# Kernel tuning notes

Hardware: AMD Instinct MI355X
Metric: run time of the kernel (lower is better)

## Reference

```python
import jax, jax.numpy as jnp
import numpy as np

N = 100000   # nodes
E = 1200000  # edges
D = 64       # emb_dim
XIN = 18     # x_dim + node_dim
XD = 16      # x_dim (output)
ED = 1       # edge_dim
L = 4        # num message-passing layers
G = 8        # graphs in batch (for global_mean_pool)


def setup_inputs() -> dict:
    key = jax.random.key(0)
    ks = iter(jax.random.split(key, 64))
    def nrm(shape, s=0.05):
        return jax.random.normal(next(ks), shape, dtype=jnp.float32) * s
    inp = {}
    inp["x"] = jax.random.normal(next(ks), (N, XIN), dtype=jnp.float32)
    inp["edge_attr"] = jax.random.normal(next(ks), (E, ED), dtype=jnp.float32)
    inp["W_in"] = nrm((XIN, D)); inp["b_in"] = jnp.zeros((D,), jnp.float32)
    # per-layer stacked params (leading dim L)
    inp["msg_W1"] = nrm((L, 2 * D + ED, D)); inp["msg_b1"] = jnp.zeros((L, D), jnp.float32)
    inp["msg_g1"] = jnp.ones((L, D), jnp.float32); inp["msg_be1"] = jnp.zeros((L, D), jnp.float32)
    inp["msg_W2"] = nrm((L, D, D)); inp["msg_b2"] = jnp.zeros((L, D), jnp.float32)
    inp["msg_g2"] = jnp.ones((L, D), jnp.float32); inp["msg_be2"] = jnp.zeros((L, D), jnp.float32)
    inp["upd_W1"] = nrm((L, 2 * D, D)); inp["upd_b1"] = jnp.zeros((L, D), jnp.float32)
    inp["upd_g1"] = jnp.ones((L, D), jnp.float32); inp["upd_be1"] = jnp.zeros((L, D), jnp.float32)
    inp["upd_W2"] = nrm((L, D, D)); inp["upd_b2"] = jnp.zeros((L, D), jnp.float32)
    inp["upd_g2"] = jnp.ones((L, D), jnp.float32); inp["upd_be2"] = jnp.zeros((L, D), jnp.float32)
    inp["reward_W"] = nrm((D, D)); inp["reward_b"] = jnp.zeros((D,), jnp.float32)
    inp["rout_W"] = nrm((D, 1)); inp["rout_b"] = jnp.zeros((1,), jnp.float32)
    inp["pred_W"] = nrm((D, D)); inp["pred_b"] = jnp.zeros((D,), jnp.float32)
    inp["pout_W"] = nrm((D, XD)); inp["pout_b"] = jnp.zeros((XD,), jnp.float32)
    inp["edge_index"] = jax.random.randint(next(ks), (2, E), 0, N)
    inp["batch"] = jnp.sort(jax.random.randint(next(ks), (N,), 0, G))
    return inp


def _bn(x, g, b, eps=1e-5):
    # BatchNorm1d in training mode: batch mean + biased variance
    m = jnp.mean(x, axis=0)
    v = jnp.mean((x - m) ** 2, axis=0)
    return (x - m) * jax.lax.rsqrt(v + eps) * g + b


def _mlp(x, W1, b1, g1, be1, W2, b2, g2, be2):
    h = jax.nn.relu(_bn(x @ W1 + b1, g1, be1))
    return jax.nn.relu(_bn(h @ W2 + b2, g2, be2))


def _forward(x, edge_attr, W_in, b_in,
             msg_W1, msg_b1, msg_g1, msg_be1, msg_W2, msg_b2, msg_g2, msg_be2,
             upd_W1, upd_b1, upd_g1, upd_be1, upd_W2, upd_b2, upd_g2, upd_be2,
             reward_W, reward_b, rout_W, rout_b, pred_W, pred_b, pout_W, pout_b,
             edge_index, batch):
    src = edge_index[0]  # j (source)
    dst = edge_index[1]  # i (target); PyG default flow source_to_target
    n = x.shape[0]
    h = x @ W_in + b_in
    for l in range(L):
        # message: gather + concat + MLP(psi)
        m = jnp.concatenate([h[dst], h[src], edge_attr], axis=-1)  # (E, 2D+ED)
        m = _mlp(m, msg_W1[l], msg_b1[l], msg_g1[l], msg_be1[l],
                 msg_W2[l], msg_b2[l], msg_g2[l], msg_be2[l])
        # aggregate: scatter-add to target nodes
        agg = jax.ops.segment_sum(m, dst, num_segments=n)  # (N, D)
        # update: concat + MLP(phi); residual add from outer network
        u = jnp.concatenate([h, agg], axis=-1)
        h = h + _mlp(u, upd_W1[l], upd_b1[l], upd_g1[l], upd_be1[l],
                     upd_W2[l], upd_b2[l], upd_g2[l], upd_be2[l])
    # reward head (computed in the original forward but not returned)
    h_reward = h @ reward_W + reward_b
    cnt = jax.ops.segment_sum(jnp.ones((n,), h.dtype), batch, num_segments=G)
    h_graph = jax.ops.segment_sum(h_reward, batch, num_segments=G) / jnp.maximum(cnt, 1.0)[:, None]
    _out_reward = h_graph @ rout_W + rout_b  # unused, matches original return
    # prediction head
    x_out = jax.nn.relu(h @ pred_W + pred_b) @ pout_W + pout_b  # (N, XD)
    return x_out


def reference(x, edge_attr, W_in, b_in,
              msg_W1, msg_b1, msg_g1, msg_be1, msg_W2, msg_b2, msg_g2, msg_be2,
              upd_W1, upd_b1, upd_g1, upd_be1, upd_W2, upd_b2, upd_g2, upd_be2,
              reward_W, reward_b, rout_W, rout_b, pred_W, pred_b, pout_W, pout_b,
              edge_index, batch):
    return _forward(x, edge_attr, W_in, b_in,
                    msg_W1, msg_b1, msg_g1, msg_be1, msg_W2, msg_b2, msg_g2, msg_be2,
                    upd_W1, upd_b1, upd_g1, upd_be1, upd_W2, upd_b2, upd_g2, upd_be2,
                    reward_W, reward_b, rout_W, rout_b, pred_W, pred_b, pout_W, pout_b,
                    edge_index, batch)
```

## Files before the change

### kernel.cpp

```cpp
#include <hip/hip_runtime.h>
#include <hip/hip_fp16.h>

typedef unsigned short u16;
typedef unsigned int u32;
typedef __attribute__((ext_vector_type(8))) unsigned short us8;
typedef __attribute__((ext_vector_type(8))) _Float16 f16x8;
typedef __attribute__((ext_vector_type(4))) float f32x4;

#define EPS 1e-5f

__device__ __forceinline__ float h2f(u16 h){ __half v; *(u16*)&v = h; return __half2float(v); }
__device__ __forceinline__ u16 f2h(float f){ __half v = __float2half(f); return *(u16*)&v; }

__global__ __launch_bounds__(256) void k_in(const float* __restrict__ x,
    const float* __restrict__ Win, const float* __restrict__ bin,
    float* __restrict__ h, int N){
  __shared__ float Ws[18][64];
  __shared__ float xs[64][20];
  int tid = threadIdx.x;
  for (int i = tid; i < 18*64; i += 256) Ws[i>>6][i&63] = Win[i];
  int row0 = blockIdx.x * 64;
  for (int i = tid; i < 64*18; i += 256){
    int r = i/18, k = i - r*18;
    int row = row0 + r;
    xs[r][k] = (row < N) ? x[(size_t)row*18 + k] : 0.f;
  }
  __syncthreads();
  int rq = tid >> 4, dq = tid & 15;
  float4 b4 = *(const float4*)(bin + dq*4);
  float acc[4][4];
  #pragma unroll
  for (int j=0;j<4;j++){ acc[j][0]=b4.x; acc[j][1]=b4.y; acc[j][2]=b4.z; acc[j][3]=b4.w; }
  for (int k=0;k<18;k++){
    float4 wv = *(const float4*)&Ws[k][dq*4];
    #pragma unroll
    for (int j=0;j<4;j++){
      float v = xs[rq*4+j][k];
      acc[j][0]+=v*wv.x; acc[j][1]+=v*wv.y; acc[j][2]+=v*wv.z; acc[j][3]+=v*wv.w;
    }
  }
  #pragma unroll
  for (int j=0;j<4;j++){
    int row = row0 + rq*4 + j;
    if (row < N)
      *(float4*)(h + (size_t)row*64 + dq*4) = make_float4(acc[j][0],acc[j][1],acc[j][2],acc[j][3]);
  }
}

__global__ __launch_bounds__(256) void k_pq(const float* __restrict__ h,
    const float* __restrict__ A, const float* __restrict__ B,
    u16* __restrict__ P, u16* __restrict__ Q, int N){
  __shared__ float hs[64][68];
  __shared__ float As[64][64];
  __shared__ float Bs[64][64];
  int tid = threadIdx.x;
  for (int i = tid; i < 4096; i += 256){ As[i>>6][i&63] = A[i]; Bs[i>>6][i&63] = B[i]; }
  int row0 = blockIdx.x*64;
  for (int i = tid; i < 4096; i += 256){
    int r = i>>6, k = i&63; int row = row0+r;
    hs[r][k] = (row<N)? h[(size_t)row*64+k] : 0.f;
  }
  __syncthreads();
  int rq = tid>>4, dq = tid&15;
  float ap[4][4]={}, aq[4][4]={};
  for (int k=0;k<64;k+=4){
    float4 hv[4];
    #pragma unroll
    for (int j=0;j<4;j++) hv[j] = *(const float4*)&hs[rq*4+j][k];
    #pragma unroll
    for (int kk=0;kk<4;kk++){
      float4 av = *(const float4*)&As[k+kk][dq*4];
      float4 bv = *(const float4*)&Bs[k+kk][dq*4];
      #pragma unroll
      for (int j=0;j<4;j++){
        float v = ((const float*)&hv[j])[kk];
        ap[j][0]+=v*av.x; ap[j][1]+=v*av.y; ap[j][2]+=v*av.z; ap[j][3]+=v*av.w;
        aq[j][0]+=v*bv.x; aq[j][1]+=v*bv.y; aq[j][2]+=v*bv.z; aq[j][3]+=v*bv.w;
      }
    }
  }
  #pragma unroll
  for (int j=0;j<4;j++){
    int row = row0 + rq*4 + j;
    if (row<N){
      ushort4 pk, qk;
      pk.x=f2h(ap[j][0]); pk.y=f2h(ap[j][1]); pk.z=f2h(ap[j][2]); pk.w=f2h(ap[j][3]);
      qk.x=f2h(aq[j][0]); qk.y=f2h(aq[j][1]); qk.z=f2h(aq[j][2]); qk.w=f2h(aq[j][3]);
      *(ushort4*)(P+(size_t)row*64+dq*4) = pk;
      *(ushort4*)(Q+(size_t)row*64+dq*4) = qk;
    }
  }
}

__global__ __launch_bounds__(256) void k_hist(const int* __restrict__ ei, int* __restrict__ cnt, int E){
  int e = blockIdx.x*256 + threadIdx.x;
  if (e < E) atomicAdd(&cnt[ei[E+e]], 1);
}

__global__ __launch_bounds__(256) void k_scan_a(const int* __restrict__ cnt, int* __restrict__ rp,
    int* __restrict__ bsum, int N){
  __shared__ int sm[256];
  int tid = threadIdx.x;
  int i0 = blockIdx.x*1024 + tid*4;
  int v0 = (i0+0<N)? cnt[i0+0]:0;
  int v1 = (i0+1<N)? cnt[i0+1]:0;
  int v2 = (i0+2<N)? cnt[i0+2]:0;
  int v3 = (i0+3<N)? cnt[i0+3]:0;
  int s = v0+v1+v2+v3;
  sm[tid] = s; __syncthreads();
  for (int ofs=1; ofs<256; ofs<<=1){
    int v = sm[tid];
    if (tid >= ofs) v += sm[tid-ofs];
    __syncthreads(); sm[tid] = v; __syncthreads();
  }
  int base = sm[tid] - s;
  int a0 = base+v0, a1 = a0+v1, a2 = a1+v2, a3 = a2+v3;
  if (i0+0<N) rp[i0+0]=a0;
  if (i0+1<N) rp[i0+1]=a1;
  if (i0+2<N) rp[i0+2]=a2;
  if (i0+3<N) rp[i0+3]=a3;
  if (tid==255) bsum[blockIdx.x] = sm[255];
}

__global__ void k_scan_b(int* __restrict__ bsum, int NB){
  if (threadIdx.x==0){
    int run = 0;
    for (int b=0;b<NB;b++){ int t = bsum[b]; bsum[b] = run; run += t; }
  }
}

__global__ __launch_bounds__(256) void k_scan_c(const int* __restrict__ cnt, int* __restrict__ rp,
    int* __restrict__ wr, const int* __restrict__ bsum, int N, int E){
  int tid = threadIdx.x;
  int i0 = blockIdx.x*1024 + tid*4;
  int off = bsum[blockIdx.x];
  #pragma unroll
  for (int j=0;j<4;j++){
    int i = i0+j;
    if (i<N){ int ex = off + rp[i] - cnt[i]; rp[i] = ex; wr[i] = ex; }
  }
  if (blockIdx.x==0 && tid==0) rp[N] = E;
}

__global__ __launch_bounds__(256) void k_perm(const int* __restrict__ ei, const float* __restrict__ ea,
    int* __restrict__ wr, int* __restrict__ srcS, float* __restrict__ eaS, int E){
  int e = blockIdx.x*256 + threadIdx.x;
  if (e < E){
    int dn = ei[E+e];
    int pos = atomicAdd(&wr[dn], 1);
    srcS[pos] = ei[e];
    eaS[pos]  = ea[e];
  }
}

__global__ __launch_bounds__(256) void k_t1s(const u16* __restrict__ P, const u16* __restrict__ Q,
    const int* __restrict__ srcS, const float* __restrict__ eaS, const int* __restrict__ rp,
    const float* __restrict__ c1, const float* __restrict__ b1,
    u16* __restrict__ t, float* __restrict__ stats, int N){
  int tid = threadIdx.x;
  int d = tid & 63, w = tid >> 6;
  float cv = c1[d], bv = b1[d];
  float s = 0.f, sq = 0.f;
  for (int n = blockIdx.x*4 + w; n < N; n += gridDim.x*4){
    int a = rp[n], b = rp[n+1];
    float pv = h2f(P[(size_t)n*64 + d]) + bv;
    int p = a;
    for (; p + 1 < b; p += 2){
      int sn0 = srcS[p], sn1 = srcS[p+1];
      float ea0 = eaS[p], ea1 = eaS[p+1];
      float q0 = h2f(Q[(size_t)sn0*64 + d]);
      float q1 = h2f(Q[(size_t)sn1*64 + d]);
      float t0 = pv + q0 + ea0*cv;
      float t1 = pv + q1 + ea1*cv;
      t[(size_t)p*64 + d] = f2h(t0);
      t[(size_t)(p+1)*64 + d] = f2h(t1);
      s += t0 + t1; sq += t0*t0 + t1*t1;
    }
    if (p < b){
      int sn = srcS[p];
      float tt = pv + h2f(Q[(size_t)sn*64 + d]) + eaS[p]*cv;
      t[(size_t)p*64 + d] = f2h(tt);
      s += tt; sq += tt*tt;
    }
  }
  __shared__ float sS[4][64], qS[4][64];
  sS[w][d] = s; qS[w][d] = sq;
  __syncthreads();
  if (tid < 64){
    float ts = sS[0][tid]+sS[1][tid]+sS[2][tid]+sS[3][tid];
    float tq = qS[0][tid]+qS[1][tid]+qS[2][tid]+qS[3][tid];
    atomicAdd(&stats[tid], ts);
    atomicAdd(&stats[64+tid], tq);
  }
}

__global__ __launch_bounds__(256) void k_m2s(u16* __restrict__ t,
    const float* __restrict__ g1, const float* __restrict__ be1, const float* __restrict__ stats1,
    const float* __restrict__ W2, const float* __restrict__ b2,
    float* __restrict__ stats2, int E, float invE){
  __shared__ _Float16 yL[64][72];
  __shared__ _Float16 wL[64][72];
  __shared__ float scS[64], shS[64], b2S[64];
  int tid = threadIdx.x;
  if (tid < 64){
    float m = stats1[tid]*invE;
    float v = stats1[64+tid]*invE - m*m;
    float sc = g1[tid]*rsqrtf(v + EPS);
    scS[tid] = sc; shS[tid] = be1[tid] - m*sc;
    b2S[tid] = b2[tid];
  }
  for (int i = tid; i < 4096; i += 256){
    int k = i >> 6, n = i & 63;
    wL[n][k] = (_Float16)W2[i];
  }
  __syncthreads();
  int lane = tid & 63, wv = tid >> 6;
  int arow = lane & 15;
  int kgrp = lane >> 4;
  int srow = tid >> 2, sc0 = (tid & 3)*16;
  float ssum[4] = {}, ssq[4] = {};
  int ntiles = (E + 63) >> 6;
  for (int tile = blockIdx.x; tile < ntiles; tile += gridDim.x){
    int e0 = tile << 6;
    {
      int p = e0 + srow;
      f16x8 v0, v1;
      if (p < E){
        f16x8 a = *(const f16x8*)(t + (size_t)p*64 + sc0);
        f16x8 b = *(const f16x8*)(t + (size_t)p*64 + sc0 + 8);
        #pragma unroll
        for (int j=0;j<8;j++) v0[j] = (_Float16)fmaxf((float)a[j]*scS[sc0+j] + shS[sc0+j], 0.f);
        #pragma unroll
        for (int j=0;j<8;j++) v1[j] = (_Float16)fmaxf((float)b[j]*scS[sc0+8+j] + shS[sc0+8+j], 0.f);
      } else {
        #pragma unroll
        for (int j=0;j<8;j++){ v0[j] = (_Float16)0.f; v1[j] = (_Float16)0.f; }
      }
      *(f16x8*)&yL[srow][sc0]     = v0;
      *(f16x8*)&yL[srow][sc0 + 8] = v1;
    }
    __syncthreads();
    f16x8 a0 = *(const f16x8*)&yL[16*wv + arow][8*kgrp];
    f16x8 a1 = *(const f16x8*)&yL[16*wv + arow][32 + 8*kgrp];
    f32x4 acc[4];
    #pragma unroll
    for (int c=0;c<4;c++){
      f16x8 b0 = *(const f16x8*)&wL[16*c + arow][8*kgrp];
      f16x8 b1 = *(const f16x8*)&wL[16*c + arow][32 + 8*kgrp];
      f32x4 d = {0.f,0.f,0.f,0.f};
      d = __builtin_amdgcn_mfma_f32_16x16x32_f16(a0, b0, d, 0, 0, 0);
      d = __builtin_amdgcn_mfma_f32_16x16x32_f16(a1, b1, d, 0, 0, 0);
      acc[c] = d;
    }
    __syncthreads();
    #pragma unroll
    for (int c=0;c<4;c++){
      int col = 16*c + arow;
      float bb = b2S[col];
      #pragma unroll
      for (int r=0;r<4;r++){
        int e = e0 + 16*wv + kgrp*4 + r;
        if (e < E){
          float v = acc[c][r] + bb;
          t[(size_t)e*64 + col] = f2h(v);
          ssum[c] += v; ssq[c] += v*v;
        }
      }
    }
  }
  __syncthreads();
  float* red = (float*)yL;
  #pragma unroll
  for (int c=0;c<4;c++) red[c*256 + tid] = ssum[c];
  __syncthreads();
  if (tid < 64){
    int cc = tid >> 4;
    float s = 0.f;
    for (int g=0; g<16; g++) s += red[cc*256 + g*16 + (tid & 15)];
    atomicAdd(&stats2[tid], s);
  }
  __syncthreads();
  #pragma unroll
  for (int c=0;c<4;c++) red[c*256 + tid] = ssq[c];
  __syncthreads();
  if (tid < 64){
    int cc = tid >> 4;
    float s = 0.f;
    for (int g=0; g<16; g++) s += red[cc*256 + g*16 + (tid & 15)];
    atomicAdd(&stats2[64+tid], s);
  }
}

__global__ __launch_bounds__(256) void k_agg(const u16* __restrict__ t2, const int* __restrict__ rp,
    const float* __restrict__ g2, const float* __restrict__ be2, const float* __restrict__ stats2,
    float* __restrict__ agg, int N, float invE){
  __shared__ float scS[64], shS[64];
  int tid = threadIdx.x;
  if (tid < 64){
    float m = stats2[tid]*invE;
    float v = stats2[64+tid]*invE - m*m;
    float sc = g2[tid]*rsqrtf(v+EPS);
    scS[tid] = sc; shS[tid] = be2[tid] - m*sc;
  }
  __syncthreads();
  int lane = tid & 63, w = tid >> 6;
  float sc = scS[lane], sh = shS[lane];
  for (int n = blockIdx.x*4 + w; n < N; n += gridDim.x*4){
    int a = rp[n], b = rp[n+1];
    float acc = 0.f;
    for (int p = a; p < b; ++p){
      float v = h2f(t2[(size_t)p*64 + lane]);
      acc += fmaxf(v*sc + sh, 0.f);
    }
    agg[(size_t)n*64 + lane] = acc;
  }
}

__global__ __launch_bounds__(256) void k_s1(const u16* __restrict__ P, const u16* __restrict__ Q,
    const float* __restrict__ ea, const int* __restrict__ ei,
    const float* __restrict__ c1, const float* __restrict__ b1,
    float* __restrict__ stats, int E){
  int tid = threadIdx.x;
  int d = tid & 63, w = tid >> 6;
  float cv = c1[d], bv = b1[d];
  float s = 0.f, sq = 0.f;
  for (int e = blockIdx.x*4 + w; e < E; e += gridDim.x*4){
    int dn = ei[E+e], sn = ei[e];
    float t = h2f(P[(size_t)dn*64+d]) + h2f(Q[(size_t)sn*64+d]) + ea[e]*cv + bv;
    s += t; sq += t*t;
  }
  __shared__ float sS[4][64], qS[4][64];
  sS[w][d] = s; qS[w][d] = sq;
  __syncthreads();
  if (tid < 64){
    float ts = sS[0][tid]+sS[1][tid]+sS[2][tid]+sS[3][tid];
    float tq = qS[0][tid]+qS[1][tid]+qS[2][tid]+qS[3][tid];
    atomicAdd(&stats[tid], ts);
    atomicAdd(&stats[64+tid], tq);
  }
}

__global__ __launch_bounds__(256) void k_m2b(const u16* __restrict__ P, const u16* __restrict__ Q,
    const float* __restrict__ ea, const int* __restrict__ ei,
    const float* __restrict__ c1, const float* __restrict__ b1,
    const float* __restrict__ g1, const float* __restrict__ be1,
    const float* __restrict__ stats1,
    const float* __restrict__ W2, const float* __restrict__ b2,
    float* __restrict__ stats2, int E, float invE){
  __shared__ float ys[64][68];
  __shared__ float Ws[64][64];
  __shared__ float scS[64], c1S[64], bS[64], b2S[64];
  int tid = threadIdx.x;
  if (tid < 64){
    float m = stats1[tid]*invE;
    float v = stats1[64+tid]*invE - m*m;
    float sc = g1[tid]*rsqrtf(v + EPS);
    float sh = be1[tid] - m*sc;
    scS[tid] = sc;
    c1S[tid] = c1[tid]*sc;
    bS[tid]  = b1[tid]*sc + sh;
    b2S[tid] = b2[tid];
  }
  for (int i=tid;i<4096;i+=256) Ws[i>>6][i&63] = W2[i];
  __syncthreads();
  int rq = tid>>4, dq = tid&15;
  float ssum[4]={}, ssq[4]={};
  int ntiles = (E+63)>>6;
  for (int tile = blockIdx.x; tile < ntiles; tile += gridDim.x){
    int e0 = tile<<6;
    for (int i = tid; i < 4096; i += 256){
      int el = i>>6, dd = i&63;
      int e = e0 + el;
      float y = 0.f;
      if (e < E){
        int dn = ei[E+e], sn = ei[e];
        float t = (h2f(P[(size_t)dn*64+dd]) + h2f(Q[(size_t)sn*64+dd]))*scS[dd] + ea[e]*c1S[dd] + bS[dd];
        y = fmaxf(t, 0.f);
      }
      ys[el][dd] = y;
    }
    __syncthreads();
    float acc[4][4];
    float4 b4 = *(const float4*)&b2S[dq*4];
    #pragma unroll
    for (int j=0;j<4;j++){ acc[j][0]=b4.x; acc[j][1]=b4.y; acc[j][2]=b4.z; acc[j][3]=b4.w; }
    for (int k=0;k<64;k+=4){
      float4 hv[4];
      #pragma unroll
      for (int j=0;j<4;j++) hv[j] = *(const float4*)&ys[rq*4+j][k];
      #pragma unroll
      for (int kk=0;kk<4;kk++){
        float4 wv = *(const float4*)&Ws[k+kk][dq*4];
        #pragma unroll
        for (int j=0;j<4;j++){
          float v = ((const float*)&hv[j])[kk];
          acc[j][0]+=v*wv.x; acc[j][1]+=v*wv.y; acc[j][2]+=v*wv.z; acc[j][3]+=v*wv.w;
        }
      }
    }
    #pragma unroll
    for (int j=0;j<4;j++){
      int e = e0 + rq*4 + j;
      if (e < E){
        #pragma unroll
        for (int c=0;c<4;c++){ float v=acc[j][c]; ssum[c]+=v; ssq[c]+=v*v; }
      }
    }
    __syncthreads();
  }
  float* red = &ys[0][0];
  #pragma unroll
  for (int c=0;c<4;c++) red[rq*64 + dq*4 + c] = ssum[c];
  __syncthreads();
  if (tid < 64){
    float t=0.f;
    for (int r=0;r<16;r++) t += red[r*64+tid];
    atomicAdd(&stats2[tid], t);
  }
  __syncthreads();
  #pragma unroll
  for (int c=0;c<4;c++) red[rq*64 + dq*4 + c] = ssq[c];
  __syncthreads();
  if (tid < 64){
    float t=0.f;
    for (int r=0;r<16;r++) t += red[r*64+tid];
    atomicAdd(&stats2[64+tid], t);
  }
}

__global__ __launch_bounds__(256) void k_sc_rec(const u16* __restrict__ P, const u16* __restrict__ Q,
    const float* __restrict__ ea, const int* __restrict__ ei,
    const float* __restrict__ c1, const float* __restrict__ b1,
    const float* __restrict__ g1, const float* __restrict__ be1, const float* __restrict__ stats1,
    const float* __restrict__ W2, const float* __restrict__ b2,
    const float* __restrict__ g2, const float* __restrict__ be2, const float* __restrict__ stats2,
    float* __restrict__ agg, int E, float invE){
  __shared__ float ys[64][68];
  __shared__ float Ws[64][64];
  __shared__ float scS[64], c1S[64], bS[64];
  __shared__ float s2S[64], h2S[64], b2S[64];
  int tid = threadIdx.x;
  if (tid < 64){
    float m = stats1[tid]*invE;
    float v = stats1[64+tid]*invE - m*m;
    float sc = g1[tid]*rsqrtf(v + EPS);
    scS[tid] = sc;
    c1S[tid] = c1[tid]*sc;
    bS[tid]  = b1[tid]*sc + be1[tid] - m*sc;
    float m2 = stats2[tid]*invE;
    float v2 = stats2[64+tid]*invE - m2*m2;
    float sc2 = g2[tid]*rsqrtf(v2+EPS);
    s2S[tid] = sc2; h2S[tid] = be2[tid] - m2*sc2;
    b2S[tid] = b2[tid];
  }
  for (int i=tid;i<4096;i+=256) Ws[i>>6][i&63] = W2[i];
  __syncthreads();
  int rq = tid>>4, dq = tid&15;
  int ntiles = (E+63)>>6;
  for (int tile = blockIdx.x; tile < ntiles; tile += gridDim.x){
    int e0 = tile<<6;
    for (int i = tid; i < 4096; i += 256){
      int el = i>>6, dd = i&63;
      int e = e0 + el;
      float y = 0.f;
      if (e < E){
        int dn = ei[E+e], sn = ei[e];
        float t = (h2f(P[(size_t)dn*64+dd]) + h2f(Q[(size_t)sn*64+dd]))*scS[dd] + ea[e]*c1S[dd] + bS[dd];
        y = fmaxf(t, 0.f);
      }
      ys[el][dd] = y;
    }
    __syncthreads();
    float acc[4][4];
    float4 b4 = *(const float4*)&b2S[dq*4];
    #pragma unroll
    for (int j=0;j<4;j++){ acc[j][0]=b4.x; acc[j][1]=b4.y; acc[j][2]=b4.z; acc[j][3]=b4.w; }
    for (int k=0;k<64;k+=4){
      float4 hv[4];
      #pragma unroll
      for (int j=0;j<4;j++) hv[j] = *(const float4*)&ys[rq*4+j][k];
      #pragma unroll
      for (int kk=0;kk<4;kk++){
        float4 wv = *(const float4*)&Ws[k+kk][dq*4];
        #pragma unroll
        for (int j=0;j<4;j++){
          float v = ((const float*)&hv[j])[kk];
          acc[j][0]+=v*wv.x; acc[j][1]+=v*wv.y; acc[j][2]+=v*wv.z; acc[j][3]+=v*wv.w;
        }
      }
    }
    float4 sc4 = *(const float4*)&s2S[dq*4];
    float4 sh4 = *(const float4*)&h2S[dq*4];
    #pragma unroll
    for (int j=0;j<4;j++){
      int e = e0 + rq*4 + j;
      if (e < E){
        int dn = ei[E+e];
        float y0 = fmaxf(acc[j][0]*sc4.x + sh4.x, 0.f);
        float y1 = fmaxf(acc[j][1]*sc4.y + sh4.y, 0.f);
        float y2 = fmaxf(acc[j][2]*sc4.z + sh4.z, 0.f);
        float y3 = fmaxf(acc[j][3]*sc4.w + sh4.w, 0.f);
        atomicAdd(&agg[(size_t)dn*64 + dq*4    ], y0);
        atomicAdd(&agg[(size_t)dn*64 + dq*4 + 1], y1);
        atomicAdd(&agg[(size_t)dn*64 + dq*4 + 2], y2);
        atomicAdd(&agg[(size_t)dn*64 + dq*4 + 3], y3);
      }
    }
    __syncthreads();
  }
}

__global__ __launch_bounds__(256) void k_up1(const float* __restrict__ h, const float* __restrict__ agg,
    const float* __restrict__ U1, const float* __restrict__ b1u,
    float* __restrict__ tn, float* __restrict__ stats3, int N){
  __shared__ float ins[64][68];
  __shared__ float Ws[64][64];
  int tid = threadIdx.x;
  int rq = tid>>4, dq = tid&15;
  int row0 = blockIdx.x*64;
  float4 b4 = *(const float4*)(b1u + dq*4);
  float acc[4][4];
  #pragma unroll
  for (int j=0;j<4;j++){ acc[j][0]=b4.x; acc[j][1]=b4.y; acc[j][2]=b4.z; acc[j][3]=b4.w; }
  for (int p=0;p<2;p++){
    const float* src = p ? agg : h;
    for (int i=tid;i<4096;i+=256){
      int r=i>>6,k=i&63; int row=row0+r;
      ins[r][k] = (row<N)? src[(size_t)row*64+k] : 0.f;
    }
    for (int i=tid;i<4096;i+=256) Ws[i>>6][i&63] = U1[p*4096 + i];
    __syncthreads();
    for (int k=0;k<64;k+=4){
      float4 hv[4];
      #pragma unroll
      for (int j=0;j<4;j++) hv[j] = *(const float4*)&ins[rq*4+j][k];
      #pragma unroll
      for (int kk=0;kk<4;kk++){
        float4 wv = *(const float4*)&Ws[k+kk][dq*4];
        #pragma unroll
        for (int j=0;j<4;j++){
          float v = ((const float*)&hv[j])[kk];
          acc[j][0]+=v*wv.x; acc[j][1]+=v*wv.y; acc[j][2]+=v*wv.z; acc[j][3]+=v*wv.w;
        }
      }
    }
    __syncthreads();
  }
  float ssum[4]={}, ssq[4]={};
  #pragma unroll
  for (int j=0;j<4;j++){
    int row = row0 + rq*4 + j;
    if (row<N){
      *(float4*)(tn+(size_t)row*64+dq*4) = make_float4(acc[j][0],acc[j][1],acc[j][2],acc[j][3]);
      #pragma unroll
      for (int c=0;c<4;c++){ float v=acc[j][c]; ssum[c]+=v; ssq[c]+=v*v; }
    }
  }
  float* red = &ins[0][0];
  #pragma unroll
  for (int c=0;c<4;c++) red[rq*64 + dq*4 + c] = ssum[c];
  __syncthreads();
  if (tid < 64){
    float t=0.f; for (int r=0;r<16;r++) t += red[r*64+tid];
    atomicAdd(&stats3[tid], t);
  }
  __syncthreads();
  #pragma unroll
  for (int c=0;c<4;c++) red[rq*64 + dq*4 + c] = ssq[c];
  __syncthreads();
  if (tid < 64){
    float t=0.f; for (int r=0;r<16;r++) t += red[r*64+tid];
    atomicAdd(&stats3[64+tid], t);
  }
}

__global__ __launch_bounds__(256) void k_up2(float* __restrict__ tn,
    const float* __restrict__ g3, const float* __restrict__ be3, const float* __restrict__ stats3,
    const float* __restrict__ U2, const float* __restrict__ b2u,
    float* __restrict__ stats4, int N, float invN){
  __shared__ float ys[64][68];
  __shared__ float Ws[64][64];
  __shared__ float scS[64], shS[64], bS[64];
  int tid = threadIdx.x;
  if (tid < 64){
    float m = stats3[tid]*invN;
    float v = stats3[64+tid]*invN - m*m;
    float sc = g3[tid]*rsqrtf(v+EPS);
    scS[tid] = sc; shS[tid] = be3[tid] - m*sc; bS[tid] = b2u[tid];
  }
  for (int i=tid;i<4096;i+=256) Ws[i>>6][i&63] = U2[i];
  int row0 = blockIdx.x*64;
  __syncthreads();
  for (int i=tid;i<4096;i+=256){
    int r=i>>6,k=i&63; int row=row0+r;
    float y = 0.f;
    if (row<N) y = fmaxf(tn[(size_t)row*64+k]*scS[k] + shS[k], 0.f);
    ys[r][k] = y;
  }
  __syncthreads();
  int rq = tid>>4, dq = tid&15;
  float4 b4 = *(const float4*)&bS[dq*4];
  float acc[4][4];
  #pragma unroll
  for (int j=0;j<4;j++){ acc[j][0]=b4.x; acc[j][1]=b4.y; acc[j][2]=b4.z; acc[j][3]=b4.w; }
  for (int k=0;k<64;k+=4){
    float4 hv[4];
    #pragma unroll
    for (int j=0;j<4;j++) hv[j] = *(const float4*)&ys[rq*4+j][k];
    #pragma unroll
    for (int kk=0;kk<4;kk++){
      float4 wv = *(const float4*)&Ws[k+kk][dq*4];
      #pragma unroll
      for (int j=0;j<4;j++){
        float v = ((const float*)&hv[j])[kk];
        acc[j][0]+=v*wv.x; acc[j][1]+=v*wv.y; acc[j][2]+=v*wv.z; acc[j][3]+=v*wv.w;
      }
    }
  }
  float ssum[4]={}, ssq[4]={};
  #pragma unroll
  for (int j=0;j<4;j++){
    int row = row0 + rq*4 + j;
    if (row<N){
      *(float4*)(tn+(size_t)row*64+dq*4) = make_float4(acc[j][0],acc[j][1],acc[j][2],acc[j][3]);
      #pragma unroll
      for (int c=0;c<4;c++){ float v=acc[j][c]; ssum[c]+=v; ssq[c]+=v*v; }
    }
  }
  __syncthreads();
  float* red = &ys[0][0];
  #pragma unroll
  for (int c=0;c<4;c++) red[rq*64 + dq*4 + c] = ssum[c];
  __syncthreads();
  if (tid < 64){
    float t=0.f; for (int r=0;r<16;r++) t += red[r*64+tid];
    atomicAdd(&stats4[tid], t);
  }
  __syncthreads();
  #pragma unroll
  for (int c=0;c<4;c++) red[rq*64 + dq*4 + c] = ssq[c];
  __syncthreads();
  if (tid < 64){
    float t=0.f; for (int r=0;r<16;r++) t += red[r*64+tid];
    atomicAdd(&stats4[64+tid], t);
  }
}

__global__ __launch_bounds__(256) void k_res_pq(float* __restrict__ h, const float* __restrict__ tn,
    const float* __restrict__ g4, const float* __restrict__ be4, const float* __restrict__ stats4,
    const float* __restrict__ A, const float* __restrict__ B,
    u16* __restrict__ P, u16* __restrict__ Q, int N, float invN){
  __shared__ float hs[64][68];
  __shared__ float As[64][64];
  __shared__ float Bs[64][64];
  __shared__ float scS[64], shS[64];
  int tid = threadIdx.x;
  if (tid < 64){
    float m = stats4[tid]*invN;
    float v = stats4[64+tid]*invN - m*m;
    float sc = g4[tid]*rsqrtf(v+EPS);
    scS[tid] = sc; shS[tid] = be4[tid] - m*sc;
  }
  for (int i = tid; i < 4096; i += 256){ As[i>>6][i&63] = A[i]; Bs[i>>6][i&63] = B[i]; }
  int row0 = blockIdx.x*64;
  __syncthreads();
  for (int i = tid; i < 4096; i += 256){
    int r = i>>6, k = i&63; int row = row0+r;
    float hv = 0.f;
    if (row<N){
      hv = h[(size_t)row*64+k] + fmaxf(tn[(size_t)row*64+k]*scS[k] + shS[k], 0.f);
      h[(size_t)row*64+k] = hv;
    }
    hs[r][k] = hv;
  }
  __syncthreads();
  int rq = tid>>4, dq = tid&15;
  float ap[4][4]={}, aq[4][4]={};
  for (int k=0;k<64;k+=4){
    float4 hv[4];
    #pragma unroll
    for (int j=0;j<4;j++) hv[j] = *(const float4*)&hs[rq*4+j][k];
    #pragma unroll
    for (int kk=0;kk<4;kk++){
      float4 av = *(const float4*)&As[k+kk][dq*4];
      float4 bv = *(const float4*)&Bs[k+kk][dq*4];
      #pragma unroll
      for (int j=0;j<4;j++){
        float v = ((const float*)&hv[j])[kk];
        ap[j][0]+=v*av.x; ap[j][1]+=v*av.y; ap[j][2]+=v*av.z; ap[j][3]+=v*av.w;
        aq[j][0]+=v*bv.x; aq[j][1]+=v*bv.y; aq[j][2]+=v*bv.z; aq[j][3]+=v*bv.w;
      }
    }
  }
  #pragma unroll
  for (int j=0;j<4;j++){
    int row = row0 + rq*4 + j;
    if (row<N){
      ushort4 pk, qk;
      pk.x=f2h(ap[j][0]); pk.y=f2h(ap[j][1]); pk.z=f2h(ap[j][2]); pk.w=f2h(ap[j][3]);
      qk.x=f2h(aq[j][0]); qk.y=f2h(aq[j][1]); qk.z=f2h(aq[j][2]); qk.w=f2h(aq[j][3]);
      *(ushort4*)(P+(size_t)row*64+dq*4) = pk;
      *(ushort4*)(Q+(size_t)row*64+dq*4) = qk;
    }
  }
}

__global__ __launch_bounds__(256) void k_res_head(const float* __restrict__ h, const float* __restrict__ tn,
    const float* __restrict__ g4, const float* __restrict__ be4, const float* __restrict__ stats4,
    const float* __restrict__ Wp, const float* __restrict__ bp,
    const float* __restrict__ Wo, const float* __restrict__ bo,
    float* __restrict__ out, int N, float invN){
  __shared__ float hs[64][68];
  __shared__ float Wps[64][64];
  __shared__ float ps[64][68];
  __shared__ float Wos[64][16];
  __shared__ float scS[64], shS[64];
  int tid = threadIdx.x;
  if (tid < 64){
    float m = stats4[tid]*invN;
    float v = stats4[64+tid]*invN - m*m;
    float sc = g4[tid]*rsqrtf(v+EPS);
    scS[tid] = sc; shS[tid] = be4[tid] - m*sc;
  }
  for (int i=tid;i<4096;i+=256) Wps[i>>6][i&63] = Wp[i];
  for (int i=tid;i<1024;i+=256) Wos[i>>4][i&15] = Wo[i];
  int row0 = blockIdx.x*64;
  __syncthreads();
  for (int i = tid; i < 4096; i += 256){
    int r = i>>6, k = i&63; int row = row0+r;
    float hv = 0.f;
    if (row<N)
      hv = h[(size_t)row*64+k] + fmaxf(tn[(size_t)row*64+k]*scS[k] + shS[k], 0.f);
    hs[r][k] = hv;
  }
  __syncthreads();
  int rq = tid>>4, dq = tid&15;
  float4 b4 = *(const float4*)(bp + dq*4);
  float acc[4][4];
  #pragma unroll
  for (int j=0;j<4;j++){ acc[j][0]=b4.x; acc[j][1]=b4.y; acc[j][2]=b4.z; acc[j][3]=b4.w; }
  for (int k=0;k<64;k+=4){
    float4 hv[4];
    #pragma unroll
    for (int j=0;j<4;j++) hv[j] = *(const float4*)&hs[rq*4+j][k];
    #pragma unroll
    for (int kk=0;kk<4;kk++){
      float4 wv = *(const float4*)&Wps[k+kk][dq*4];
      #pragma unroll
      for (int j=0;j<4;j++){
        float v = ((const float*)&hv[j])[kk];
        acc[j][0]+=v*wv.x; acc[j][1]+=v*wv.y; acc[j][2]+=v*wv.z; acc[j][3]+=v*wv.w;
      }
    }
  }
  #pragma unroll
  for (int j=0;j<4;j++){
    *(float4*)&ps[rq*4+j][dq*4] = make_float4(fmaxf(acc[j][0],0.f), fmaxf(acc[j][1],0.f),
                                              fmaxf(acc[j][2],0.f), fmaxf(acc[j][3],0.f));
  }
  __syncthreads();
  int f = tid & 15;
  float bof = bo[f];
  float acc2[4] = {bof, bof, bof, bof};
  for (int k=0;k<64;k++){
    float wv = Wos[k][f];
    #pragma unroll
    for (int j=0;j<4;j++) acc2[j] += ps[rq*4+j][k]*wv;
  }
  #pragma unroll
  for (int j=0;j<4;j++){
    int row = row0 + rq*4 + j;
    if (row<N) out[(size_t)row*16 + f] = acc2[j];
  }
}

extern "C" void kernel_launch(void* const* d_in, const int* in_sizes, int n_in,
                              void* d_out, int out_size, void* d_ws, size_t ws_size,
                              hipStream_t stream){
  const float* x    = (const float*)d_in[0];
  const float* eatt = (const float*)d_in[1];
  const float* Win  = (const float*)d_in[2];
  const float* bin  = (const float*)d_in[3];
  const float* mW1  = (const float*)d_in[4];
  const float* mb1  = (const float*)d_in[5];
  const float* mg1  = (const float*)d_in[6];
  const float* mbe1 = (const float*)d_in[7];
  const float* mW2  = (const float*)d_in[8];
  const float* mb2  = (const float*)d_in[9];
  const float* mg2  = (const float*)d_in[10];
  const float* mbe2 = (const float*)d_in[11];
  const float* uW1  = (const float*)d_in[12];
  const float* ub1  = (const float*)d_in[13];
  const float* ug1  = (const float*)d_in[14];
  const float* ube1 = (const float*)d_in[15];
  const float* uW2  = (const float*)d_in[16];
  const float* ub2  = (const float*)d_in[17];
  const float* ug2  = (const float*)d_in[18];
  const float* ube2 = (const float*)d_in[19];
  const float* predW = (const float*)d_in[24];
  const float* predb = (const float*)d_in[25];
  const float* poutW = (const float*)d_in[26];
  const float* poutb = (const float*)d_in[27];
  const int*   ei    = (const int*)d_in[28];

  const int N = in_sizes[0] / 18;
  const int E = in_sizes[1];

  size_t nodeB = (size_t)N * 64 * sizeof(float);
  size_t halfB = (size_t)N * 64 * sizeof(u16);
  size_t t2B   = (size_t)E * 64 * sizeof(u16);
  size_t statsB = 16 * 128 * sizeof(float);
  int NB = (N + 1023)/1024;
  size_t csrB = (size_t)E*4 + (size_t)E*4 + (size_t)(N+1)*4 + (size_t)N*4 + (size_t)N*4 + 4096*4;

  bool planA = ws_size >= nodeB + 2*halfB + nodeB + t2B + csrB + statsB;

  char* w = (char*)d_ws;
  float* h = (float*)w; w += nodeB;
  u16* P = (u16*)w; w += halfB;
  u16* Q = (u16*)w; w += halfB;
  float* agg = (float*)w; w += nodeB;
  float* tn = agg;
  u16*  t2 = nullptr;
  int *srcS=nullptr, *rp=nullptr, *cnt=nullptr, *wrp=nullptr, *bsum=nullptr;
  float* eaS=nullptr;
  float* stats;
  if (planA){
    t2   = (u16*)w;  w += t2B;
    srcS = (int*)w;  w += (size_t)E*4;
    eaS  = (float*)w; w += (size_t)E*4;
    rp   = (int*)w;  w += (size_t)(N+1)*4;
    cnt  = (int*)w;  w += (size_t)N*4;
    wrp  = (int*)w;  w += (size_t)N*4;
    bsum = (int*)w;  w += 4096*4;
    stats = (float*)w;
  } else {
    stats = (float*)w;
  }

  hipMemsetAsync(stats, 0, statsB, stream);

  int nb = (N + 63)/64;
  float invE = 1.0f/(float)E, invN = 1.0f/(float)N;

  k_in<<<nb, 256, 0, stream>>>(x, Win, bin, h, N);
  k_pq<<<nb, 256, 0, stream>>>(h, mW1, mW1 + 4096, P, Q, N);

  if (planA){
    hipMemsetAsync(cnt, 0, (size_t)N*4, stream);
    k_hist<<<(E+255)/256, 256, 0, stream>>>(ei, cnt, E);
    k_scan_a<<<NB, 256, 0, stream>>>(cnt, rp, bsum, N);
    k_scan_b<<<1, 64, 0, stream>>>(bsum, NB);
    k_scan_c<<<NB, 256, 0, stream>>>(cnt, rp, wrp, bsum, N, E);
    k_perm<<<(E+255)/256, 256, 0, stream>>>(ei, eatt, wrp, srcS, eaS, E);
  }

  for (int l = 0; l < 4; ++l){
    float* s1 = stats + (l*4+0)*128;
    float* s2 = stats + (l*4+1)*128;
    float* s3 = stats + (l*4+2)*128;
    float* s4 = stats + (l*4+3)*128;
    const float* A  = mW1 + (size_t)l*8256;
    const float* c1 = A + 8192;
    if (planA){
      k_t1s<<<2048, 256, 0, stream>>>(P, Q, srcS, eaS, rp, c1, mb1 + l*64, t2, s1, N);
      k_m2s<<<2048, 256, 0, stream>>>(t2, mg1 + l*64, mbe1 + l*64, s1,
                                      mW2 + (size_t)l*4096, mb2 + l*64, s2, E, invE);
      k_agg<<<2048, 256, 0, stream>>>(t2, rp, mg2 + l*64, mbe2 + l*64, s2, agg, N, invE);
    } else {
      k_s1<<<2048, 256, 0, stream>>>(P, Q, eatt, ei, c1, mb1 + l*64, s1, E);
      k_m2b<<<1024, 256, 0, stream>>>(P, Q, eatt, ei, c1, mb1 + l*64, mg1 + l*64, mbe1 + l*64,
                                      s1, mW2 + (size_t)l*4096, mb2 + l*64, s2, E, invE);
      hipMemsetAsync(agg, 0, nodeB, stream);
      k_sc_rec<<<1024, 256, 0, stream>>>(P, Q, eatt, ei, c1, mb1 + l*64, mg1 + l*64, mbe1 + l*64,
                                         s1, mW2 + (size_t)l*4096, mb2 + l*64,
                                         mg2 + l*64, mbe2 + l*64, s2, agg, E, invE);
    }
    k_up1<<<nb, 256, 0, stream>>>(h, agg, uW1 + (size_t)l*8192, ub1 + l*64, tn, s3, N);
    k_up2<<<nb, 256, 0, stream>>>(tn, ug1 + l*64, ube1 + l*64, s3, uW2 + (size_t)l*4096,
                                  ub2 + l*64, s4, N, invN);
    if (l < 3){
      const float* An = mW1 + (size_t)(l+1)*8256;
      k_res_pq<<<nb, 256, 0, stream>>>(h, tn, ug2 + l*64, ube2 + l*64, s4,
                                       An, An + 4096, P, Q, N, invN);
    } else {
      k_res_head<<<nb, 256, 0, stream>>>(h, tn, ug2 + l*64, ube2 + l*64, s4,
                                         predW, predb, poutW, poutb, (float*)d_out, N, invN);
    }
  }
}
```

Baseline: 2.284 ms.

## Pack edge src/attr, widen per-lane loads in edge kernels, double m2s tile

Packs source index and edge attribute into one int2 array so the CSR gather reads one 8-byte record per edge. In k_t1s and k_agg each lane now handles two feature channels with 32-bit loads and stores, and the two half-wavefronts process alternating edges, combined with a shuffle in k_agg. k_m2s processes 128-edge tiles with two MFMA row fragments per wave, amortising the weight fragment loads and barriers. The cost is more registers and LDS in k_m2s, and it changes the per-lane reduction layout.

```diff
diff --git a/kernel.cpp b/kernel.cpp
--- a/kernel.cpp
+++ b/kernel.cpp
@@ -143,52 +143,66 @@
 }
 
 __global__ __launch_bounds__(256) void k_perm(const int* __restrict__ ei, const float* __restrict__ ea,
-    int* __restrict__ wr, int* __restrict__ srcS, float* __restrict__ eaS, int E){
+    int* __restrict__ wr, int2* __restrict__ seS, int E){
   int e = blockIdx.x*256 + threadIdx.x;
   if (e < E){
     int dn = ei[E+e];
     int pos = atomicAdd(&wr[dn], 1);
-    srcS[pos] = ei[e];
-    eaS[pos]  = ea[e];
+    seS[pos] = make_int2(ei[e], __float_as_int(ea[e]));
   }
 }
 
 __global__ __launch_bounds__(256) void k_t1s(const u16* __restrict__ P, const u16* __restrict__ Q,
-    const int* __restrict__ srcS, const float* __restrict__ eaS, const int* __restrict__ rp,
+    const int2* __restrict__ seS, const int* __restrict__ rp,
     const float* __restrict__ c1, const float* __restrict__ b1,
     u16* __restrict__ t, float* __restrict__ stats, int N){
   int tid = threadIdx.x;
-  int d = tid & 63, w = tid >> 6;
-  float cv = c1[d], bv = b1[d];
-  float s = 0.f, sq = 0.f;
+  int lane = tid & 63, w = tid >> 6;
+  int sub = lane >> 5;
+  int dl = (lane & 31) * 2;
+  float cv0 = c1[dl], cv1 = c1[dl+1];
+  float bv0 = b1[dl], bv1 = b1[dl+1];
+  float s0 = 0.f, s1 = 0.f, qs0 = 0.f, qs1 = 0.f;
   for (int n = blockIdx.x*4 + w; n < N; n += gridDim.x*4){
     int a = rp[n], b = rp[n+1];
-    float pv = h2f(P[(size_t)n*64 + d]) + bv;
-    int p = a;
-    for (; p + 1 < b; p += 2){
-      int sn0 = srcS[p], sn1 = srcS[p+1];
-      float ea0 = eaS[p], ea1 = eaS[p+1];
-      float q0 = h2f(Q[(size_t)sn0*64 + d]);
-      float q1 = h2f(Q[(size_t)sn1*64 + d]);
-      float t0 = pv + q0 + ea0*cv;
-      float t1 = pv + q1 + ea1*cv;
-      t[(size_t)p*64 + d] = f2h(t0);
-      t[(size_t)(p+1)*64 + d] = f2h(t1);
-      s += t0 + t1; sq += t0*t0 + t1*t1;
-    }
-    if (p < b){
-      int sn = srcS[p];
-      float tt = pv + h2f(Q[(size_t)sn*64 + d]) + eaS[p]*cv;
-      t[(size_t)p*64 + d] = f2h(tt);
-      s += tt; sq += tt*tt;
-    }
-  }
-  __shared__ float sS[4][64], qS[4][64];
-  sS[w][d] = s; qS[w][d] = sq;
-  __syncthreads();
-  if (tid < 64){
-    float ts = sS[0][tid]+sS[1][tid]+sS[2][tid]+sS[3][tid];
-    float tq = qS[0][tid]+qS[1][tid]+qS[2][tid]+qS[3][tid];
+    u32 pp = *(const u32*)(P + (size_t)n*64 + dl);
+    float p0 = h2f((u16)(pp & 0xffffu)) + bv0;
+    float p1 = h2f((u16)(pp >> 16)) + bv1;
+    int p = a + sub;
+    for (; p + 2 < b; p += 4){
+      int2 seA = seS[p];
+      int2 seB = seS[p+2];
+      u32 qA = *(const u32*)(Q + (size_t)seA.x*64 + dl);
+      u32 qB = *(const u32*)(Q + (size_t)seB.x*64 + dl);
+      float eaA = __int_as_float(seA.y), eaB = __int_as_float(seB.y);
+      float tA0 = p0 + h2f((u16)(qA & 0xffffu)) + eaA*cv0;
+      float tA1 = p1 + h2f((u16)(qA >> 16)) + eaA*cv1;
+      float tB0 = p0 + h2f((u16)(qB & 0xffffu)) + eaB*cv0;
+      float tB1 = p1 + h2f((u16)(qB >> 16)) + eaB*cv1;
+      *(u32*)(t + (size_t)p*64 + dl) = (u32)f2h(tA0) | ((u32)f2h(tA1) << 16);
+      *(u32*)(t + (size_t)(p+2)*64 + dl) = (u32)f2h(tB0) | ((u32)f2h(tB1) << 16);
+      s0 += tA0 + tB0; s1 += tA1 + tB1;
+      qs0 += tA0*tA0 + tB0*tB0; qs1 += tA1*tA1 + tB1*tB1;
+    }
+    for (; p < b; p += 2){
+      int2 se = seS[p];
+      u32 qq = *(const u32*)(Q + (size_t)se.x*64 + dl);
+      float ea = __int_as_float(se.y);
+      float t0 = p0 + h2f((u16)(qq & 0xffffu)) + ea*cv0;
+      float t1 = p1 + h2f((u16)(qq >> 16)) + ea*cv1;
+      *(u32*)(t + (size_t)p*64 + dl) = (u32)f2h(t0) | ((u32)f2h(t1) << 16);
+      s0 += t0; s1 += t1; qs0 += t0*t0; qs1 += t1*t1;
+    }
+  }
+  __shared__ float sS[8][64], qS[8][64];
+  int idx = w*2 + sub;
+  sS[idx][dl] = s0; sS[idx][dl+1] = s1;
+  qS[idx][dl] = qs0; qS[idx][dl+1] = qs1;
+  __syncthreads();
+  if (tid < 64){
+    float ts = 0.f, tq = 0.f;
+    #pragma unroll
+    for (int r=0;r<8;r++){ ts += sS[r][tid]; tq += qS[r][tid]; }
     atomicAdd(&stats[tid], ts);
     atomicAdd(&stats[64+tid], tq);
   }
@@ -198,7 +212,7 @@
     const float* __restrict__ g1, const float* __restrict__ be1, const float* __restrict__ stats1,
     const float* __restrict__ W2, const float* __restrict__ b2,
     float* __restrict__ stats2, int E, float invE){
-  __shared__ _Float16 yL[64][72];
+  __shared__ _Float16 yL[128][72];
   __shared__ _Float16 wL[64][72];
   __shared__ float scS[64], shS[64], b2S[64];
   int tid = threadIdx.x;
@@ -217,53 +231,66 @@
   int lane = tid & 63, wv = tid >> 6;
   int arow = lane & 15;
   int kgrp = lane >> 4;
-  int srow = tid >> 2, sc0 = (tid & 3)*16;
+  int srow = tid >> 1, sc0 = (tid & 1)*32;
   float ssum[4] = {}, ssq[4] = {};
-  int ntiles = (E + 63) >> 6;
+  int ntiles = (E + 127) >> 7;
   for (int tile = blockIdx.x; tile < ntiles; tile += gridDim.x){
-    int e0 = tile << 6;
+    int e0 = tile << 7;
     {
       int p = e0 + srow;
-      f16x8 v0, v1;
       if (p < E){
-        f16x8 a = *(const f16x8*)(t + (size_t)p*64 + sc0);
-        f16x8 b = *(const f16x8*)(t + (size_t)p*64 + sc0 + 8);
+        const u16* src = t + (size_t)p*64 + sc0;
         #pragma unroll
-        for (int j=0;j<8;j++) v0[j] = (_Float16)fmaxf((float)a[j]*scS[sc0+j] + shS[sc0+j], 0.f);
+        for (int c=0;c<4;c++){
+          f16x8 a = *(const f16x8*)(src + c*8);
+          f16x8 v;
+          #pragma unroll
+          for (int j=0;j<8;j++){
+            int dd = sc0 + c*8 + j;
+            v[j] = (_Float16)fmaxf((float)a[j]*scS[dd] + shS[dd], 0.f);
+          }
+          *(f16x8*)&yL[srow][sc0 + c*8] = v;
+        }
+      } else {
+        f16x8 z;
         #pragma unroll
-        for (int j=0;j<8;j++) v1[j] = (_Float16)fmaxf((float)b[j]*scS[sc0+8+j] + shS[sc0+8+j], 0.f);
-      } else {
+        for (int j=0;j<8;j++) z[j] = (_Float16)0.f;
         #pragma unroll
-        for (int j=0;j<8;j++){ v0[j] = (_Float16)0.f; v1[j] = (_Float16)0.f; }
-      }
-      *(f16x8*)&yL[srow][sc0]     = v0;
-      *(f16x8*)&yL[srow][sc0 + 8] = v1;
+        for (int c=0;c<4;c++) *(f16x8*)&yL[srow][sc0 + c*8] = z;
+      }
     }
     __syncthreads();
-    f16x8 a0 = *(const f16x8*)&yL[16*wv + arow][8*kgrp];
-    f16x8 a1 = *(const f16x8*)&yL[16*wv + arow][32 + 8*kgrp];
-    f32x4 acc[4];
-    #pragma unroll
-    for (int c=0;c<4;c++){
-      f16x8 b0 = *(const f16x8*)&wL[16*c + arow][8*kgrp];
-      f16x8 b1 = *(const f16x8*)&wL[16*c + arow][32 + 8*kgrp];
-      f32x4 d = {0.f,0.f,0.f,0.f};
-      d = __builtin_amdgcn_mfma_f32_16x16x32_f16(a0, b0, d, 0, 0, 0);
-      d = __builtin_amdgcn_mfma_f32_16x16x32_f16(a1, b1, d, 0, 0, 0);
-      acc[c] = d;
+    f32x4 acc[2][4];
+    #pragma unroll
+    for (int mf=0; mf<2; mf++){
+      int row = 32*wv + 16*mf + arow;
+      f16x8 a0 = *(const f16x8*)&yL[row][8*kgrp];
+      f16x8 a1 = *(const f16x8*)&yL[row][32 + 8*kgrp];
+      #pragma unroll
+      for (int c=0;c<4;c++){
+        f16x8 b0 = *(const f16x8*)&wL[16*c + arow][8*kgrp];
+        f16x8 b1 = *(const f16x8*)&wL[16*c + arow][32 + 8*kgrp];
+        f32x4 d = {0.f,0.f,0.f,0.f};
+        d = __builtin_amdgcn_mfma_f32_16x16x32_f16(a0, b0, d, 0, 0, 0);
+        d = __builtin_amdgcn_mfma_f32_16x16x32_f16(a1, b1, d, 0, 0, 0);
+        acc[mf][c] = d;
+      }
     }
     __syncthreads();
     #pragma unroll
-    for (int c=0;c<4;c++){
-      int col = 16*c + arow;
-      float bb = b2S[col];
-      #pragma unroll
-      for (int r=0;r<4;r++){
-        int e = e0 + 16*wv + kgrp*4 + r;
-        if (e < E){
-          float v = acc[c][r] + bb;
-          t[(size_t)e*64 + col] = f2h(v);
-          ssum[c] += v; ssq[c] += v*v;
+    for (int mf=0; mf<2; mf++){
+      #pragma unroll
+      for (int c=0;c<4;c++){
+        int col = 16*c + arow;
+        float bb = b2S[col];
+        #pragma unroll
+        for (int r=0;r<4;r++){
+          int e = e0 + 32*wv + 16*mf + 4*kgrp + r;
+          if (e < E){
+            float v = acc[mf][c][r] + bb;
+            t[(size_t)e*64 + col] = f2h(v);
+            ssum[c] += v; ssq[c] += v*v;
+          }
         }
       }
     }
@@ -304,15 +331,30 @@
   }
   __syncthreads();
   int lane = tid & 63, w = tid >> 6;
-  float sc = scS[lane], sh = shS[lane];
+  int sub = lane >> 5;
+  int dl = (lane & 31) * 2;
+  float sc0 = scS[dl], sc1 = scS[dl+1], sh0 = shS[dl], sh1 = shS[dl+1];
   for (int n = blockIdx.x*4 + w; n < N; n += gridDim.x*4){
     int a = rp[n], b = rp[n+1];
-    float acc = 0.f;
-    for (int p = a; p < b; ++p){
-      float v = h2f(t2[(size_t)p*64 + lane]);
-      acc += fmaxf(v*sc + sh, 0.f);
-    }
-    agg[(size_t)n*64 + lane] = acc;
+    float a0 = 0.f, a1 = 0.f;
+    int p = a + sub;
+    for (; p + 2 < b; p += 4){
+      u32 vA = *(const u32*)(t2 + (size_t)p*64 + dl);
+      u32 vB = *(const u32*)(t2 + (size_t)(p+2)*64 + dl);
+      a0 += fmaxf(h2f((u16)(vA & 0xffffu))*sc0 + sh0, 0.f)
+          + fmaxf(h2f((u16)(vB & 0xffffu))*sc0 + sh0, 0.f);
+      a1 += fmaxf(h2f((u16)(vA >> 16))*sc1 + sh1, 0.f)
+          + fmaxf(h2f((u16)(vB >> 16))*sc1 + sh1, 0.f);
+    }
+    for (; p < b; p += 2){
+      u32 vA = *(const u32*)(t2 + (size_t)p*64 + dl);
+      a0 += fmaxf(h2f((u16)(vA & 0xffffu))*sc0 + sh0, 0.f);
+      a1 += fmaxf(h2f((u16)(vA >> 16))*sc1 + sh1, 0.f);
+    }
+    a0 += __shfl_xor(a0, 32);
+    a1 += __shfl_xor(a1, 32);
+    if (sub == 0)
+      *(float2*)(agg + (size_t)n*64 + dl) = make_float2(a0, a1);
   }
 }
 
@@ -811,7 +853,7 @@
   size_t t2B   = (size_t)E * 64 * sizeof(u16);
   size_t statsB = 16 * 128 * sizeof(float);
   int NB = (N + 1023)/1024;
-  size_t csrB = (size_t)E*4 + (size_t)E*4 + (size_t)(N+1)*4 + (size_t)N*4 + (size_t)N*4 + 4096*4;
+  size_t csrB = (size_t)E*8 + (size_t)(N+1)*4 + (size_t)N*4 + (size_t)N*4 + 4096*4;
 
   bool planA = ws_size >= nodeB + 2*halfB + nodeB + t2B + csrB + statsB;
 
@@ -822,13 +864,12 @@
   float* agg = (float*)w; w += nodeB;
   float* tn = agg;
   u16*  t2 = nullptr;
-  int *srcS=nullptr, *rp=nullptr, *cnt=nullptr, *wrp=nullptr, *bsum=nullptr;
-  float* eaS=nullptr;
+  int2* seS = nullptr;
+  int *rp=nullptr, *cnt=nullptr, *wrp=nullptr, *bsum=nullptr;
   float* stats;
   if (planA){
     t2   = (u16*)w;  w += t2B;
-    srcS = (int*)w;  w += (size_t)E*4;
-    eaS  = (float*)w; w += (size_t)E*4;
+    seS  = (int2*)w; w += (size_t)E*8;
     rp   = (int*)w;  w += (size_t)(N+1)*4;
     cnt  = (int*)w;  w += (size_t)N*4;
     wrp  = (int*)w;  w += (size_t)N*4;
@@ -852,7 +893,7 @@
     k_scan_a<<<NB, 256, 0, stream>>>(cnt, rp, bsum, N);
     k_scan_b<<<1, 64, 0, stream>>>(bsum, NB);
     k_scan_c<<<NB, 256, 0, stream>>>(cnt, rp, wrp, bsum, N, E);
-    k_perm<<<(E+255)/256, 256, 0, stream>>>(ei, eatt, wrp, srcS, eaS, E);
+    k_perm<<<(E+255)/256, 256, 0, stream>>>(ei, eatt, wrp, seS, E);
   }
 
   for (int l = 0; l < 4; ++l){
@@ -863,7 +904,7 @@
     const float* A  = mW1 + (size_t)l*8256;
     const float* c1 = A + 8192;
     if (planA){
-      k_t1s<<<2048, 256, 0, stream>>>(P, Q, srcS, eaS, rp, c1, mb1 + l*64, t2, s1, N);
+      k_t1s<<<2048, 256, 0, stream>>>(P, Q, seS, rp, c1, mb1 + l*64, t2, s1, N);
       k_m2s<<<2048, 256, 0, stream>>>(t2, mg1 + l*64, mbe1 + l*64, s1,
                                       mW2 + (size_t)l*4096, mb2 + l*64, s2, E, invE);
       k_agg<<<2048, 256, 0, stream>>>(t2, rp, mg2 + l*64, mbe2 + l*64, s2, agg, N, invE);
```

Result: faster. 2.166 ms (-5.2%).
